# Kernel optimization log

Hardware: AMD Instinct MI355X
Metric: run time of the kernel (lower is better)

The kernel has to match this reference:

```python
import jax, jax.numpy as jnp
import numpy as np

E = 200_000   # edges (messages)
T = 2_000_000 # triplets
N = 20_000    # atoms/nodes
H = 128       # hidden_channels
INT = 64      # int_emb_size
BAS = 8       # basis_emb_size
OUT_EMB = 256 # out_emb_channels
NRAD = 6
SBF_DIM = 7 * 6  # num_spherical * num_radial = 42
NB = 4        # num_blocks
OUTC = 1      # num_targets


def setup_inputs() -> dict:
    key = jax.random.key(0)
    ks = iter(jax.random.split(key, 64))

    def w(shape):
        # glorot-ish scaled weights, stored as [in, out] for x @ W
        return jax.random.normal(next(ks), shape, jnp.float32) / np.sqrt(shape[-2])

    return dict(
        x=jax.random.normal(next(ks), (E, H), jnp.float32),
        rbf=jax.random.normal(next(ks), (E, NRAD), jnp.float32),
        sbf=jax.random.normal(next(ks), (T, SBF_DIM), jnp.float32),
        # interaction block params, stacked over NB blocks
        W_rbf1=w((NB, NRAD, BAS)), W_rbf2=w((NB, BAS, H)),
        W_sbf1=w((NB, SBF_DIM, BAS)), W_sbf2=w((NB, BAS, INT)),
        W_kj=w((NB, H, H)), b_kj=jnp.zeros((NB, H), jnp.float32),
        W_ji=w((NB, H, H)), b_ji=jnp.zeros((NB, H), jnp.float32),
        W_down=w((NB, H, INT)), W_up=w((NB, INT, H)),
        Wb=w((NB, 2, H, H)), bb=jnp.zeros((NB, 2, H), jnp.float32),   # num_before_skip=1 -> 2 linears
        Wa=w((NB, 4, H, H)), ba=jnp.zeros((NB, 4, H), jnp.float32),   # num_after_skip=2 -> 4 linears
        W_lin=w((NB, H, H)), b_lin=jnp.zeros((NB, H), jnp.float32),
        # output block params, stacked over NB+1 blocks
        Wo_rbf=w((NB + 1, NRAD, H)),
        Wo_up=w((NB + 1, H, OUT_EMB)), bo_up=jnp.zeros((NB + 1, OUT_EMB), jnp.float32),
        Wo_lins=w((NB + 1, 3, OUT_EMB, OUT_EMB)), bo_lins=jnp.zeros((NB + 1, 3, OUT_EMB), jnp.float32),
        Wo_out=w((NB + 1, OUT_EMB, OUTC)),
        idx_kj=jax.random.randint(next(ks), (T,), 0, E, jnp.int32),
        idx_ji=jax.random.randint(next(ks), (T,), 0, E, jnp.int32),
        idx_i=jax.random.randint(next(ks), (E,), 0, N, jnp.int32),
        num_nodes=N,
    )


def _interaction(b, x, rbf, sbf, idx_kj, idx_ji, p):
    act = jax.nn.silu
    x_ji = act(x @ p['W_ji'][b] + p['b_ji'][b])
    x_kj = act(x @ p['W_kj'][b] + p['b_kj'][b])
    rbf_t = (rbf @ p['W_rbf1'][b]) @ p['W_rbf2'][b]          # [E,H]
    x_kj = act((x_kj * rbf_t) @ p['W_down'][b])              # [E,INT]
    sbf_t = (sbf @ p['W_sbf1'][b]) @ p['W_sbf2'][b]          # [T,INT]
    m = x_kj[idx_kj] * sbf_t                                  # triplet gather [T,INT]
    agg = jax.ops.segment_sum(m, idx_ji, num_segments=x.shape[0])  # scatter-add [E,INT]
    x_kj = act(agg @ p['W_up'][b])                            # [E,H]
    h = x_ji + x_kj
    # residual layers before skip (1 layer = 2 linears)
    h = h + act(act(h @ p['Wb'][b, 0] + p['bb'][b, 0]) @ p['Wb'][b, 1] + p['bb'][b, 1])
    h = act(h @ p['W_lin'][b] + p['b_lin'][b]) + x
    # residual layers after skip (2 layers = 4 linears)
    for l in range(2):
        h = h + act(act(h @ p['Wa'][b, 2 * l] + p['ba'][b, 2 * l]) @ p['Wa'][b, 2 * l + 1] + p['ba'][b, 2 * l + 1])
    return h


def _output(b, x, rbf, idx_i, num_nodes, p):
    act = jax.nn.silu
    t = (rbf @ p['Wo_rbf'][b]) * x                            # [E,H]
    t = jax.ops.segment_sum(t, idx_i, num_segments=num_nodes) # [N,H]
    t = t @ p['Wo_up'][b] + p['bo_up'][b]
    for l in range(3):
        t = act(t @ p['Wo_lins'][b, l] + p['bo_lins'][b, l])
    return t @ p['Wo_out'][b]                                 # [N,OUTC]


def reference(x, rbf, sbf, W_rbf1, W_rbf2, W_sbf1, W_sbf2, W_kj, b_kj, W_ji, b_ji,
              W_down, W_up, Wb, bb, Wa, ba, W_lin, b_lin,
              Wo_rbf, Wo_up, bo_up, Wo_lins, bo_lins, Wo_out,
              idx_kj, idx_ji, idx_i, num_nodes):
    p = dict(W_rbf1=W_rbf1, W_rbf2=W_rbf2, W_sbf1=W_sbf1, W_sbf2=W_sbf2,
             W_kj=W_kj, b_kj=b_kj, W_ji=W_ji, b_ji=b_ji, W_down=W_down, W_up=W_up,
             Wb=Wb, bb=bb, Wa=Wa, ba=ba, W_lin=W_lin, b_lin=b_lin,
             Wo_rbf=Wo_rbf, Wo_up=Wo_up, bo_up=bo_up,
             Wo_lins=Wo_lins, bo_lins=bo_lins, Wo_out=Wo_out)
    P = _output(0, x, rbf, idx_i, num_nodes, p)
    for b in range(NB):  # fixed small layer loop
        x = _interaction(b, x, rbf, sbf, idx_kj, idx_ji, p)
        P = P + _output(b + 1, x, rbf, idx_i, num_nodes, p)
    return P
```

## Files before the change

kernel.cpp:

```cpp
#include <hip/hip_runtime.h>
#include <hip/hip_bf16.h>

#define E_EDGES 200000
#define T_TRIP  2000000
#define N_NODES 20000
#define H_DIM   128
#define INT_DIM 64
#define BAS     8
#define OUT_EMB 256
#define NRAD    6
#define SBF_D   42
#define NB      4

typedef __attribute__((ext_vector_type(8))) __bf16 bf16x8;
typedef __attribute__((ext_vector_type(4))) float f32x4;
typedef unsigned short u16;

__device__ __forceinline__ float silu_f(float v) { return v / (1.0f + __expf(-v)); }

__device__ __forceinline__ u16 f2bf(float f) {
    unsigned int u = __float_as_uint(f);
    u += 0x7FFF + ((u >> 16) & 1);
    return (u16)(u >> 16);
}
// ... 75 lines not shown
{
    __builtin_amdgcn_s_setprio(1);
    #pragma unroll
    for (int m = 0; m < 2; ++m) {
        int row = wm * 32 + m * 16 + l15;
        int off = (row * 256 + (k0 + khalf) * 2) ^ ((row & 7) << 4);
        bf16x8 ah = *reinterpret_cast<const bf16x8*>(AH + off);
        bf16x8 al = *reinterpret_cast<const bf16x8*>(AL + off);
        #pragma unroll
        for (int n = 0; n < 4; ++n) {
            acc[m][n] = __builtin_amdgcn_mfma_f32_16x16x32_bf16(b.h[n], ah, acc[m][n], 0, 0, 0);
            acc[m][n] = __builtin_amdgcn_mfma_f32_16x16x32_bf16(b.h[n], al, acc[m][n], 0, 0, 0);
            acc[m][n] = __builtin_amdgcn_mfma_f32_16x16x32_bf16(b.l[n], ah, acc[m][n], 0, 0, 0);
        }
    }
    __builtin_amdgcn_s_setprio(0);
}
__device__ __forceinline__ void mfma_cluster_T(
    const char* T, int k0, int wm, int l15, int khalf,
    const BF8x4& b, f32x4 acc[2][4])
{
    __builtin_amdgcn_s_setprio(1);
    #pragma unroll
    for (int m = 0; m < 2; ++m) {
        int row = wm * 32 + m * 16 + l15;
        int off = (row * 256 + (k0 + khalf) * 2) ^ ((row & 7) << 4);
        bf16x8 a = *reinterpret_cast<const bf16x8*>(T + off);
        #pragma unroll
        for (int n = 0; n < 4; ++n) {
            acc[m][n] = __builtin_amdgcn_mfma_f32_16x16x32_bf16(b.h[n], a, acc[m][n], 0, 0, 0);
            acc[m][n] = __builtin_amdgcn_mfma_f32_16x16x32_bf16(b.l[n], a, acc[m][n], 0, 0, 0);
        }
    }
    __builtin_amdgcn_s_setprio(0);
}
__device__ __forceinline__ void mfma_cluster64_T(
    const char* T, int k0, int wm, int l15, int khalf,
    const BF8x4& b, f32x4 acc[2][4])
{
    __builtin_amdgcn_s_setprio(1);
    #pragma unroll
    for (int m = 0; m < 2; ++m) {
        int row = wm * 32 + m * 16 + l15;
        int off = (row * 128 + (k0 + khalf) * 2) ^ ((row & 7) << 4);
        bf16x8 a = *reinterpret_cast<const bf16x8*>(T + off);
        #pragma unroll
        for (int n = 0; n < 4; ++n) {
            acc[m][n] = __builtin_amdgcn_mfma_f32_16x16x32_bf16(b.h[n], a, acc[m][n], 0, 0, 0);
            acc[m][n] = __builtin_amdgcn_mfma_f32_16x16x32_bf16(b.l[n], a, acc[m][n], 0, 0, 0);
        }
    }
    __builtin_amdgcn_s_setprio(0);
}
__device__ __forceinline__ void mfma_cluster512(
    const char* AH, const char* AL, int k0, int l15, int khalf,
    const BF8x4& b, f32x4 acc[2][4])
{
    __builtin_amdgcn_s_setprio(1);
    #pragma unroll
    for (int m = 0; m < 2; ++m) {
        int row = m * 16 + l15;
        int off = (row * 512 + (k0 + khalf) * 2) ^ ((row & 7) << 4);
        bf16x8 ah = *reinterpret_cast<const bf16x8*>(AH + off);
        bf16x8 al = *reinterpret_cast<const bf16x8*>(AL + off);
        #pragma unroll
        for (int n = 0; n < 4; ++n) {
            acc[m][n] = __builtin_amdgcn_mfma_f32_16x16x32_bf16(b.h[n], ah, acc[m][n], 0, 0, 0);
            acc[m][n] = __builtin_amdgcn_mfma_f32_16x16x32_bf16(b.h[n], al, acc[m][n], 0, 0, 0);
            acc[m][n] = __builtin_amdgcn_mfma_f32_16x16x32_bf16(b.l[n], ah, acc[m][n], 0, 0, 0);
        }
    }
    __builtin_amdgcn_s_setprio(0);
}
__device__ __forceinline__ void mfma_cluster512_T(
    const char* T, int k0, int l15, int khalf,
    const BF8x4& b, f32x4 acc[2][4])
{
    __builtin_amdgcn_s_setprio(1);
    #pragma unroll
    for (int m = 0; m < 2; ++m) {
        int row = m * 16 + l15;
        int off = (row * 512 + (k0 + khalf) * 2) ^ ((row & 7) << 4);
        bf16x8 a = *reinterpret_cast<const bf16x8*>(T + off);
        #pragma unroll
        for (int n = 0; n < 4; ++n) {
            acc[m][n] = __builtin_amdgcn_mfma_f32_16x16x32_bf16(b.h[n], a, acc[m][n], 0, 0, 0);
            acc[m][n] = __builtin_amdgcn_mfma_f32_16x16x32_bf16(b.l[n], a, acc[m][n], 0, 0, 0);
        }
    }
    __builtin_amdgcn_s_setprio(0);
}

__device__ __forceinline__ void mm128_pipe(
    const char* AH, const char* AL,
    const u16* __restrict__ Bh, const u16* __restrict__ Bl, BF8x4& pre,
    const u16* __restrict__ nBh, const u16* __restrict__ nBl,
    int wm, int wn, int l15, int khalf, f32x4 acc[2][4])
{
    BF8x4 c0 = pre;
    BF8x4 c1 = loadB128f(Bh, Bl, 32, wn, l15, khalf);
    mfma_cluster(AH, AL, 0, wm, l15, khalf, c0, acc);
    BF8x4 c2 = loadB128f(Bh, Bl, 64, wn, l15, khalf);
    mfma_cluster(AH, AL, 32, wm, l15, khalf, c1, acc);
    BF8x4 c3 = loadB128f(Bh, Bl, 96, wn, l15, khalf);
    mfma_cluster(AH, AL, 64, wm, l15, khalf, c2, acc);
    if (nBh) pre = loadB128f(nBh, nBl, 0, wn, l15, khalf);
    mfma_cluster(AH, AL, 96, wm, l15, khalf, c3, acc);
}
__device__ __forceinline__ void mm128_pipe_T(
    const char* T,
    const u16* __restrict__ Bh, const u16* __restrict__ Bl, BF8x4& pre,
    const u16* __restrict__ nBh, const u16* __restrict__ nBl,
    int wm, int wn, int l15, int khalf, f32x4 acc[2][4])
{
    BF8x4 c0 = pre;
    BF8x4 c1 = loadB128f(Bh, Bl, 32, wn, l15, khalf);
    mfma_cluster_T(T, 0, wm, l15, khalf, c0, acc);
    BF8x4 c2 = loadB128f(Bh, Bl, 64, wn, l15, khalf);
    mfma_cluster_T(T, 32, wm, l15, khalf, c1, acc);
    BF8x4 c3 = loadB128f(Bh, Bl, 96, wn, l15, khalf);
    mfma_cluster_T(T, 64, wm, l15, khalf, c2, acc);
    if (nBh) pre = loadB128f(nBh, nBl, 0, wn, l15, khalf);
    mfma_cluster_T(T, 96, wm, l15, khalf, c3, acc);
}
__device__ __forceinline__ void mm64_pipe_T(
    const char* T,
    const u16* __restrict__ Bh, const u16* __restrict__ Bl, BF8x4& pre,
    const u16* __restrict__ nBh, const u16* __restrict__ nBl,
    int wm, int wn, int l15, int khalf, f32x4 acc[2][4])
{
    BF8x4 c0 = pre;
    BF8x4 c1 = loadB64f(Bh, Bl, 32, wn, l15, khalf);
    mfma_cluster64_T(T, 0, wm, l15, khalf, c0, acc);
    if (nBh) pre = loadB128f(nBh, nBl, 0, wn, l15, khalf);
    mfma_cluster64_T(T, 32, wm, l15, khalf, c1, acc);
}

__global__ __launch_bounds__(256) void wprep(
    const float* __restrict__ src, u16* __restrict__ hi,
    u16* __restrict__ lo, int K, int N)
{
    int e = blockIdx.x * 256 + threadIdx.x;
    int total = K * N;
    if (e >= total) return;
    size_t base = (size_t)blockIdx.y * total;
    float a = src[base + e];
    int k = e / N, n = e - k * N;
    u16 h = f2bf(a);
    u16 l = f2bf(a - bf2f(h));
    hi[base + (size_t)n * K + k] = h;
    lo[base + (size_t)n * K + k] = l;
}

__global__ __launch_bounds__(256, 2) void pre_fuse(
    const float* __restrict__ X, const float* __restrict__ rbf,
    const float* __restrict__ W1,
    const u16* __restrict__ Wjih, const u16* __restrict__ Wjil, const float* __restrict__ bji,
    const u16* __restrict__ Wkjh, const u16* __restrict__ Wkjl, const float* __restrict__ bkj,
    const float* __restrict__ Wr2,
    const u16* __restrict__ Wdnh, const u16* __restrict__ Wdnl,
    u16* __restrict__ E1, u16* __restrict__ C1)
{
    __shared__ char smem[49152];
    char* XH = smem;
    char* XL = smem + 16384;
    char* IT = smem + 32768;

    const int tid  = threadIdx.x;
    const int lane = tid & 63;
    const int w    = tid >> 6;
    const int wm   = w >> 1, wn = w & 1;
    const int bm   = blockIdx.x * 64;
    const int l15  = lane & 15;
    const int khalf = (lane >> 4) * 8;
    const int r4   = (lane >> 4) * 4;

    BF8x4 pre = loadB128f(Wjih, Wjil, 0, wn, l15, khalf);

    {
        int r  = tid >> 2;
        int c0 = (tid & 3) * 32;
        const float* p = &X[(size_t)(bm + r) * H_DIM + c0];
        const int swz = (r & 7) << 4;
        #pragma unroll
        for (int q = 0; q < 8; ++q) {
            float4 f = *reinterpret_cast<const float4*>(p + q * 4);
            float vv[4] = {f.x, f.y, f.z, f.w};
            u16 h[4], l[4];
            #pragma unroll
            for (int j = 0; j < 4; ++j) {
                h[j] = f2bf(vv[j]);
                l[j] = f2bf(vv[j] - bf2f(h[j]));
            }
            int off = (r * 256 + c0 * 2 + q * 8) ^ swz;
            *reinterpret_cast<ushort4*>(XH + off) = make_ushort4(h[0], h[1], h[2], h[3]);
            *reinterpret_cast<ushort4*>(XL + off) = make_ushort4(l[0], l[1], l[2], l[3]);
        }
    }
    __syncthreads();

    {
        f32x4 acc[2][4] = {};
        mm128_pipe(XH, XL, Wjih, Wjil, pre, Wkjh, Wkjl, wm, wn, l15, khalf, acc);
        #pragma unroll
        for (int n = 0; n < 4; ++n) {
            int col0 = wn * 64 + n * 16 + r4;
            float4 bv = *reinterpret_cast<const float4*>(&bji[col0]);
            #pragma unroll
            for (int m = 0; m < 2; ++m) {
                int row = wm * 32 + m * 16 + l15;
                ushort4 ob;
                ob.x = f2bf(silu_f(acc[m][n][0] + bv.x));
                ob.y = f2bf(silu_f(acc[m][n][1] + bv.y));
                ob.z = f2bf(silu_f(acc[m][n][2] + bv.z));
                ob.w = f2bf(silu_f(acc[m][n][3] + bv.w));
                *reinterpret_cast<ushort4*>(&E1[(size_t)(bm + row) * H_DIM + col0]) = ob;
            }
        }
    }
    {
        f32x4 acc[2][4] = {};
        mm128_pipe(XH, XL, Wkjh, Wkjl, pre, nullptr, nullptr, wm, wn, l15, khalf, acc);
        float r8v[2][8];
        #pragma unroll
        for (int m = 0; m < 2; ++m) {
            int grow = bm + wm * 32 + m * 16 + l15;
            const float2* rp = reinterpret_cast<const float2*>(&rbf[(size_t)grow * NRAD]);
            float2 q0 = rp[0], q1 = rp[1], q2 = rp[2];
            float rv[NRAD] = {q0.x, q0.y, q1.x, q1.y, q2.x, q2.y};
            #pragma unroll
            for (int j = 0; j < 8; ++j) r8v[m][j] = 0.f;
            #pragma unroll
            for (int k = 0; k < NRAD; ++k)
                #pragma unroll
                for (int j = 0; j < 8; ++j)
                    r8v[m][j] = fmaf(rv[k], W1[k * BAS + j], r8v[m][j]);
        }
        #pragma unroll
        for (int n = 0; n < 4; ++n) {
            int col0 = wn * 64 + n * 16 + r4;
            float4 bvf = *reinterpret_cast<const float4*>(&bkj[col0]);
            float bv[4] = {bvf.x, bvf.y, bvf.z, bvf.w};
            float wrv[8][4];
            #pragma unroll
            for (int j = 0; j < 8; ++j) {
                float4 wf = *reinterpret_cast<const float4*>(&Wr2[j * H_DIM + col0]);
                wrv[j][0] = wf.x; wrv[j][1] = wf.y; wrv[j][2] = wf.z; wrv[j][3] = wf.w;
            }
            #pragma unroll
            for (int m = 0; m < 2; ++m) {
                int row = wm * 32 + m * 16 + l15;
                float v[4];
                #pragma unroll
                for (int r = 0; r < 4; ++r) {
                    float t = silu_f(acc[m][n][r] + bv[r]);
                    float g = 0.f;
                    #pragma unroll
                    for (int j = 0; j < 8; ++j)
                        g = fmaf(r8v[m][j], wrv[j][r], g);
                    v[r] = t * g;
                }
                st_bf4(IT, row, col0, 256, v);
            }
        }
    }
    __syncthreads();

    {
        f32x4 acc[2][2] = {};
        #pragma unroll
        for (int k0 = 0; k0 < 128; k0 += 32) {
            bf16x8 bh[2], bl[2];
            #pragma unroll
            for (int n = 0; n < 2; ++n) {
                size_t bo = (size_t)(wn * 32 + n * 16 + l15) * 128 + k0 + khalf;
                bh[n] = *reinterpret_cast<const bf16x8*>(Wdnh + bo);
                bl[n] = *reinterpret_cast<const bf16x8*>(Wdnl + bo);
            }
            __builtin_amdgcn_s_setprio(1);
            #pragma unroll
            for (int m = 0; m < 2; ++m) {
                int row = wm * 32 + m * 16 + l15;
                int off = (row * 256 + (k0 + khalf) * 2) ^ ((row & 7) << 4);
                bf16x8 a = *reinterpret_cast<const bf16x8*>(IT + off);
                #pragma unroll
                for (int n = 0; n < 2; ++n) {
                    acc[m][n] = __builtin_amdgcn_mfma_f32_16x16x32_bf16(bh[n], a, acc[m][n], 0, 0, 0);
                    acc[m][n] = __builtin_amdgcn_mfma_f32_16x16x32_bf16(bl[n], a, acc[m][n], 0, 0, 0);
                }
            }
            __builtin_amdgcn_s_setprio(0);
        }
        #pragma unroll
        for (int n = 0; n < 2; ++n) {
            int col0 = wn * 32 + n * 16 + r4;
            #pragma unroll
            for (int m = 0; m < 2; ++m) {
                int row = wm * 32 + m * 16 + l15;
                ushort4 ob;
                ob.x = f2bf(silu_f(acc[m][n][0]));
                ob.y = f2bf(silu_f(acc[m][n][1]));
                ob.z = f2bf(silu_f(acc[m][n][2]));
                ob.w = f2bf(silu_f(acc[m][n][3]));
                *reinterpret_cast<ushort4*>(&C1[(size_t)(bm + row) * INT_DIM + col0]) = ob;
            }
        }
    }
}

struct ChainP {
    const u16 *uph, *upl;
    const u16 *b0h, *b0l, *b1h, *b1l;
    const u16 *lnh, *lnl;
    const u16 *a0h, *a0l, *a1h, *a1l, *a2h, *a2l, *a3h, *a3l;
    const float *bb0, *bb1, *blin, *ba0, *ba1, *ba2, *ba3;
};
struct OutP {
    const float* TN;
    const u16 *Uh, *Ul; const float* bu;
    const u16 *L0h, *L0l; const float* b0;
    const u16 *L1h, *L1l; const float* b1;
    const u16 *L2h, *L2l; const float* b2;
    const float* Wo; float* P;
};

__device__ __forceinline__ void post_chain_body(
    char* smem, int bx,
    const u16* __restrict__ AGG, const u16* __restrict__ E1,
    const float* __restrict__ X, const ChainP& p, float* __restrict__ OUT)
{
    char* SH  = smem;
    char* SL  = smem + 16384;
    char* TMP = smem + 32768;
    char* GB  = TMP;

    const int tid  = threadIdx.x;
    const int lane = tid & 63;
    const int w    = tid >> 6;
    const int wm   = w >> 1, wn = w & 1;
    const int bm   = bx * 64;
    const int l15  = lane & 15;
    const int khalf = (lane >> 4) * 8;
    const int r4   = (lane >> 4) * 4;

    BF8x4 pre = loadB64f(p.uph, p.upl, 0, wn, l15, khalf);

    {
        int r  = tid >> 2;
        int c0 = (tid & 3) * 16;
        const ushort4* pg = reinterpret_cast<const ushort4*>(&AGG[(size_t)(bm + r) * INT_DIM + c0]);
        const int swz = (r & 7) << 4;
        #pragma unroll
        for (int q = 0; q < 4; ++q) {
            ushort4 v = pg[q];
            int off = (r * 128 + c0 * 2 + q * 8) ^ swz;
            *reinterpret_cast<ushort4*>(GB + off) = v;
        }
    }
    __syncthreads();

    f32x4 acc[2][4];
    #define ZACC { _Pragma("unroll") for (int m = 0; m < 2; ++m) \
                   _Pragma("unroll") for (int n = 0; n < 4; ++n) \
                       acc[m][n] = f32x4{0.f, 0.f, 0.f, 0.f}; }

    ZACC
    mm64_pipe_T(GB, p.uph, p.upl, pre, p.b0h, p.b0l, wm, wn, l15, khalf, acc);
    #pragma unroll
    for (int n = 0; n < 4; ++n) {
        int col0 = wn * 64 + n * 16 + r4;
        #pragma unroll
        for (int m = 0; m < 2; ++m) {
            int row = wm * 32 + m * 16 + l15;
            ushort4 e = *reinterpret_cast<const ushort4*>(&E1[(size_t)(bm + row) * H_DIM + col0]);
            float v[4];
            v[0] = bf2f(e.x) + silu_f(acc[m][n][0]);
            v[1] = bf2f(e.y) + silu_f(acc[m][n][1]);
            v[2] = bf2f(e.z) + silu_f(acc[m][n][2]);
            v[3] = bf2f(e.w) + silu_f(acc[m][n][3]);
            st_split4(SH, SL, row, col0, 256, v);
        }
    }
    __syncthreads();

    #define STAGE_PLAIN(WH, WL, BIAS, NWH, NWL)                                         \
    {                                                                                   \
        ZACC                                                                            \
        mm128_pipe(SH, SL, WH, WL, pre, NWH, NWL, wm, wn, l15, khalf, acc);             \
        _Pragma("unroll")                                                               \
        for (int n = 0; n < 4; ++n) {                                                   \
            int col0 = wn * 64 + n * 16 + r4;                                           \
            float4 bv = *reinterpret_cast<const float4*>(&BIAS[col0]);                  \
            _Pragma("unroll")                                                           \
            for (int m = 0; m < 2; ++m) {                                               \
                int row = wm * 32 + m * 16 + l15;                                       \
                float v[4];                                                             \
                v[0] = silu_f(acc[m][n][0] + bv.x);                                     \
                v[1] = silu_f(acc[m][n][1] + bv.y);                                     \
                v[2] = silu_f(acc[m][n][2] + bv.z);                                     \
                v[3] = silu_f(acc[m][n][3] + bv.w);                                     \
                st_bf4(TMP, row, col0, 256, v);                                         \
            }                                                                           \
        }                                                                               \
        __syncthreads();                                                                \
    }

    #define STAGE_RES(WH, WL, BIAS, NWH, NWL)                                           \
    {                                                                                   \
        ZACC                                                                            \
        mm128_pipe_T(TMP, WH, WL, pre, NWH, NWL, wm, wn, l15, khalf, acc);              \
        _Pragma("unroll")                                                               \
        for (int n = 0; n < 4; ++n) {                                                   \
            int col0 = wn * 64 + n * 16 + r4;                                           \
            float4 bv = *reinterpret_cast<const float4*>(&BIAS[col0]);                  \
            _Pragma("unroll")                                                           \
            for (int m = 0; m < 2; ++m) {                                               \
                int row = wm * 32 + m * 16 + l15;                                       \
                float v[4];                                                             \
                ld_split4(SH, SL, row, col0, 256, v);                                   \
                v[0] += silu_f(acc[m][n][0] + bv.x);                                    \
                v[1] += silu_f(acc[m][n][1] + bv.y);                                    \
                v[2] += silu_f(acc[m][n][2] + bv.z);                                    \
                v[3] += silu_f(acc[m][n][3] + bv.w);                                    \
                st_split4(SH, SL, row, col0, 256, v);                                   \
            }                                                                           \
        }                                                                               \
        __syncthreads();                                                                \
    }

    STAGE_PLAIN(p.b0h, p.b0l, p.bb0, p.b1h, p.b1l)
    STAGE_RES(p.b1h, p.b1l, p.bb1, p.lnh, p.lnl)

    {
        ZACC
        mm128_pipe(SH, SL, p.lnh, p.lnl, pre, p.a0h, p.a0l, wm, wn, l15, khalf, acc);
        __syncthreads();
        #pragma unroll
        for (int n = 0; n < 4; ++n) {
            int col0 = wn * 64 + n * 16 + r4;
            float4 bv = *reinterpret_cast<const float4*>(&p.blin[col0]);
            #pragma unroll
            for (int m = 0; m < 2; ++m) {
                int row = wm * 32 + m * 16 + l15;
                float4 xv = *reinterpret_cast<const float4*>(&X[(size_t)(bm + row) * H_DIM + col0]);
                float v[4];
                v[0] = silu_f(acc[m][n][0] + bv.x) + xv.x;
                v[1] = silu_f(acc[m][n][1] + bv.y) + xv.y;
                v[2] = silu_f(acc[m][n][2] + bv.z) + xv.z;
                v[3] = silu_f(acc[m][n][3] + bv.w) + xv.w;
                st_split4(SH, SL, row, col0, 256, v);
            }
        }
        __syncthreads();
    }

    STAGE_PLAIN(p.a0h, p.a0l, p.ba0, p.a1h, p.a1l)
    STAGE_RES(p.a1h, p.a1l, p.ba1, p.a2h, p.a2l)
    STAGE_PLAIN(p.a2h, p.a2l, p.ba2, p.a3h, p.a3l)

    {
        ZACC
        mm128_pipe_T(TMP, p.a3h, p.a3l, pre, nullptr, nullptr, wm, wn, l15, khalf, acc);
        #pragma unroll
        for (int n = 0; n < 4; ++n) {
            int col0 = wn * 64 + n * 16 + r4;
            float4 bv = *reinterpret_cast<const float4*>(&p.ba3[col0]);
            #pragma unroll
            for (int m = 0; m < 2; ++m) {
                int row = wm * 32 + m * 16 + l15;
                float v[4];
                ld_split4(SH, SL, row, col0, 256, v);
                float4 o;
                o.x = v[0] + silu_f(acc[m][n][0] + bv.x);
                o.y = v[1] + silu_f(acc[m][n][1] + bv.y);
                o.z = v[2] + silu_f(acc[m][n][2] + bv.z);
                o.w = v[3] + silu_f(acc[m][n][3] + bv.w);
                *reinterpret_cast<float4*>(&OUT[(size_t)(bm + row) * H_DIM + col0]) = o;
            }
        }
    }
    #undef STAGE_PLAIN
    #undef STAGE_RES
    #undef ZACC
}

__device__ __forceinline__ void out_chain_body(char* smem, int bx, const OutP& o)
{
    char* SH  = smem;
    char* SL  = smem + 16384;
    char* TMP = smem + 32768;
    char* XH  = TMP;
    char* XL  = TMP + 8192;

    const int tid  = threadIdx.x;
    const int lane = tid & 63;
    const int wn   = tid >> 6;
    const int bm   = bx * 32;
    const int l15  = lane & 15;
    const int khalf = (lane >> 4) * 8;
    const int r4   = (lane >> 4) * 4;

    {
        int r  = tid >> 3;
        int c0 = (tid & 7) * 16;
        const float* p = &o.TN[(size_t)(bm + r) * H_DIM + c0];
        const int swz = (r & 7) << 4;
        #pragma unroll
        for (int q = 0; q < 4; ++q) {
            float4 f = *reinterpret_cast<const float4*>(p + q * 4);
            float vv[4] = {f.x, f.y, f.z, f.w};
            u16 h[4], l[4];
            #pragma unroll
            for (int j = 0; j < 4; ++j) {
                h[j] = f2bf(vv[j]);
                l[j] = f2bf(vv[j] - bf2f(h[j]));
            }
            int off = (r * 256 + c0 * 2 + q * 8) ^ swz;
            *reinterpret_cast<ushort4*>(XH + off) = make_ushort4(h[0], h[1], h[2], h[3]);
            *reinterpret_cast<ushort4*>(XL + off) = make_ushort4(l[0], l[1], l[2], l[3]);
        }
    }
    __syncthreads();

    f32x4 acc[2][4];
    #define ZACC { _Pragma("unroll") for (int m = 0; m < 2; ++m) \
                   _Pragma("unroll") for (int n = 0; n < 4; ++n) \
                       acc[m][n] = f32x4{0.f, 0.f, 0.f, 0.f}; }

    {
        ZACC
        BF8x4 cur = loadB128f(o.Uh, o.Ul, 0, wn, l15, khalf);
        #pragma unroll
        for (int k = 0; k < 4; ++k) {
            BF8x4 nxt;
            if (k < 3) nxt = loadB128f(o.Uh, o.Ul, 32 * (k + 1), wn, l15, khalf);
            mfma_cluster(XH, XL, 32 * k, 0, l15, khalf, cur, acc);
            if (k < 3) cur = nxt;
        }
        __syncthreads();
        #pragma unroll
        for (int n = 0; n < 4; ++n) {
            int col0 = wn * 64 + n * 16 + r4;
            float4 bv = *reinterpret_cast<const float4*>(&o.bu[col0]);
            #pragma unroll
            for (int m = 0; m < 2; ++m) {
                int row = m * 16 + l15;
                float v[4] = {acc[m][n][0] + bv.x, acc[m][n][1] + bv.y,
                              acc[m][n][2] + bv.z, acc[m][n][3] + bv.w};
                st_split4(SH, SL, row, col0, 512, v);
            }
        }
        __syncthreads();
    }

    {
        ZACC
        BF8x4 cur = loadB256f(o.L0h, o.L0l, 0, wn, l15, khalf);
        #pragma unroll
        for (int k = 0; k < 8; ++k) {
            BF8x4 nxt;
            if (k < 7) nxt = loadB256f(o.L0h, o.L0l, 32 * (k + 1), wn, l15, khalf);
            mfma_cluster512(SH, SL, 32 * k, l15, khalf, cur, acc);
            if (k < 7) cur = nxt;
        }
        #pragma unroll
        for (int n = 0; n < 4; ++n) {
            int col0 = wn * 64 + n * 16 + r4;
            float4 bv = *reinterpret_cast<const float4*>(&o.b0[col0]);
            #pragma unroll
            for (int m = 0; m < 2; ++m) {
                int row = m * 16 + l15;
                float v[4];
                v[0] = silu_f(acc[m][n][0] + bv.x);
                v[1] = silu_f(acc[m][n][1] + bv.y);
                v[2] = silu_f(acc[m][n][2] + bv.z);
                v[3] = silu_f(acc[m][n][3] + bv.w);
                st_bf4(TMP, row, col0, 512, v);
            }
        }
        __syncthreads();
    }

    {
        ZACC
        BF8x4 cur = loadB256f(o.L1h, o.L1l, 0, wn, l15, khalf);
        #pragma unroll
        for (int k = 0; k < 8; ++k) {
            BF8x4 nxt;
            if (k < 7) nxt = loadB256f(o.L1h, o.L1l, 32 * (k + 1), wn, l15, khalf);
            mfma_cluster512_T(TMP, 32 * k, l15, khalf, cur, acc);
            if (k < 7) cur = nxt;
        }
        #pragma unroll
        for (int n = 0; n < 4; ++n) {
            int col0 = wn * 64 + n * 16 + r4;
            float4 bv = *reinterpret_cast<const float4*>(&o.b1[col0]);
            #pragma unroll
            for (int m = 0; m < 2; ++m) {
                int row = m * 16 + l15;
                float v[4];
                v[0] = silu_f(acc[m][n][0] + bv.x);
                v[1] = silu_f(acc[m][n][1] + bv.y);
                v[2] = silu_f(acc[m][n][2] + bv.z);
                v[3] = silu_f(acc[m][n][3] + bv.w);
                st_split4(SH, SL, row, col0, 512, v);
            }
        }
        __syncthreads();
    }

    {
        ZACC
        BF8x4 cur = loadB256f(o.L2h, o.L2l, 0, wn, l15, khalf);
        #pragma unroll
        for (int k = 0; k < 8; ++k) {
            BF8x4 nxt;
            if (k < 7) nxt = loadB256f(o.L2h, o.L2l, 32 * (k + 1), wn, l15, khalf);
            mfma_cluster512(SH, SL, 32 * k, l15, khalf, cur, acc);
            if (k < 7) cur = nxt;
        }
        __syncthreads();
        #pragma unroll
        for (int n = 0; n < 4; ++n) {
            int col0 = wn * 64 + n * 16 + r4;
            float4 bv = *reinterpret_cast<const float4*>(&o.b2[col0]);
            #pragma unroll
            for (int m = 0; m < 2; ++m) {
                int row = m * 16 + l15;
                float v[4];
                v[0] = silu_f(acc[m][n][0] + bv.x);
                v[1] = silu_f(acc[m][n][1] + bv.y);
                v[2] = silu_f(acc[m][n][2] + bv.z);
                v[3] = silu_f(acc[m][n][3] + bv.w);
                st_split4(SH, SL, row, col0, 512, v);
            }
        }
        __syncthreads();
    }

    {
        int row  = tid >> 3;
        int part = tid & 7;
        float s = 0.f;
        int cbase = part * 32;
        #pragma unroll
        for (int c4 = 0; c4 < 32; c4 += 4) {
            float v[4];
            ld_split4(SH, SL, row, cbase + c4, 512, v);
            float4 wv = *reinterpret_cast<const float4*>(&o.Wo[cbase + c4]);
            s = fmaf(v[0], wv.x, s);
            s = fmaf(v[1], wv.y, s);
            s = fmaf(v[2], wv.z, s);
            s = fmaf(v[3], wv.w, s);
        }
        s += __shfl_xor(s, 1);
        s += __shfl_xor(s, 2);
        s += __shfl_xor(s, 4);
        if (part == 0) o.P[bm + row] += s;
    }
    #undef ZACC
}

__global__ __launch_bounds__(256, 2) void post_fused(
    int npost,
    const u16* __restrict__ AGG, const u16* __restrict__ E1,
    const float* __restrict__ X, ChainP p, float* __restrict__ OUT, OutP o)
{
    __shared__ char smem[49152];
    if ((int)blockIdx.x < npost)
        post_chain_body(smem, blockIdx.x, AGG, E1, X, p, OUT);
    else
        out_chain_body(smem, blockIdx.x - npost, o);
}

__device__ __forceinline__ float dot8_bf(uint4 r, const float* w2) {
    float s;
    s  = bf2f((u16)(r.x)) * w2[0] + bf2f((u16)(r.x >> 16)) * w2[1];
    s += bf2f((u16)(r.y)) * w2[2] + bf2f((u16)(r.y >> 16)) * w2[3];
    s += bf2f((u16)(r.z)) * w2[4] + bf2f((u16)(r.z >> 16)) * w2[5];
    s += bf2f((u16)(r.w)) * w2[6] + bf2f((u16)(r.w >> 16)) * w2[7];
    return s;
}

__device__ __forceinline__ void triplet_body(
    int bx, int nblk,
    const u16* __restrict__ ps8b, const float* __restrict__ Wsb2,
    const u16* __restrict__ xkj, const int* __restrict__ pkj,
    const int* __restrict__ tptr, const int* __restrict__ tcnt,
    u16* __restrict__ agg)
{
    const int lane = threadIdx.x & 63;
    int wid = bx * 4 + (threadIdx.x >> 6);
    const int nw = nblk * 4;
    float w2[BAS];
    #pragma unroll
    for (int j = 0; j < BAS; ++j) w2[j] = Wsb2[j * INT_DIM + lane];

    for (int e = wid; e < E_EDGES; e += nw) {
        int start = tptr[e];
        int end   = start + tcnt[e];
        float acc0 = 0.f, acc1 = 0.f;
        int i = start;
        for (; i + 1 < end; i += 2) {
            uint4 ra = *reinterpret_cast<const uint4*>(&ps8b[(size_t)i * BAS]);
            uint4 rb = *reinterpret_cast<const uint4*>(&ps8b[(size_t)(i + 1) * BAS]);
            int e0 = pkj[i], e1 = pkj[i + 1];
            float s0 = dot8_bf(ra, w2);
            float s1 = dot8_bf(rb, w2);
            acc0 = fmaf(bf2f(xkj[(size_t)e0 * INT_DIM + lane]), s0, acc0);
            acc1 = fmaf(bf2f(xkj[(size_t)e1 * INT_DIM + lane]), s1, acc1);
        }
        if (i < end) {
            uint4 ra = *reinterpret_cast<const uint4*>(&ps8b[(size_t)i * BAS]);
            int e0 = pkj[i];
            acc0 = fmaf(bf2f(xkj[(size_t)e0 * INT_DIM + lane]), dot8_bf(ra, w2), acc0);
        }
        agg[(size_t)e * INT_DIM + lane] = f2bf(acc0 + acc1);
    }
}

__device__ __forceinline__ void out_gather_body(
    int bx, int nblk,
    const float* __restrict__ rbf, const float* __restrict__ Wor,
    const float* __restrict__ x,
    const int* __restrict__ eptr, const int* __restrict__ ecnt,
    const int* __restrict__ eperm, float* __restrict__ tN)
{
    const int lane = threadIdx.x & 63;
    int wid = bx * 4 + (threadIdx.x >> 6);
    const int nw = nblk * 4;
    float wr0[NRAD], wr1[NRAD];
    #pragma unroll
    for (int k = 0; k < NRAD; ++k) {
        wr0[k] = Wor[k * H_DIM + lane];
        wr1[k] = Wor[k * H_DIM + lane + 64];
    }
    for (int n = wid; n < N_NODES; n += nw) {
        int start = eptr[n];
        int end   = start + ecnt[n];
        float a0 = 0.f, a1 = 0.f;
        for (int i = start; i < end; ++i) {
            int e = eperm[i];
            const float2* rp = reinterpret_cast<const float2*>(&rbf[(size_t)e * NRAD]);
            float2 r0 = rp[0], r1 = rp[1], r2 = rp[2];
            float rA = r0.x*wr0[0] + r0.y*wr0[1] + r1.x*wr0[2]
                     + r1.y*wr0[3] + r2.x*wr0[4] + r2.y*wr0[5];
            float rB = r0.x*wr1[0] + r0.y*wr1[1] + r1.x*wr1[2]
                     + r1.y*wr1[3] + r2.x*wr1[4] + r2.y*wr1[5];
            a0 = fmaf(rA, x[(size_t)e * H_DIM + lane], a0);
            a1 = fmaf(rB, x[(size_t)e * H_DIM + lane + 64], a1);
        }
        tN[(size_t)n * H_DIM + lane] = a0;
        tN[(size_t)n * H_DIM + lane + 64] = a1;
    }
}

__global__ __launch_bounds__(256) void gather_fused(
    int GT,
    const u16* __restrict__ ps8b, const float* __restrict__ Wsb2,
    const u16* __restrict__ xkj, const int* __restrict__ pkj,
    const int* __restrict__ tptr, const int* __restrict__ tcnt,
    u16* __restrict__ agg,
    const float* __restrict__ rbf, const float* __restrict__ Wor,
    const float* __restrict__ x,
    const int* __restrict__ eptr, const int* __restrict__ ecnt,
    const int* __restrict__ eperm, float* __restrict__ tN)
{
    int bx = blockIdx.x;
    if (bx < GT)
        triplet_body(bx, GT, ps8b, Wsb2, xkj, pkj, tptr, tcnt, agg);
    else
        out_gather_body(bx - GT, gridDim.x - GT, rbf, Wor, x, eptr, ecnt, eperm, tN);
}

__global__ __launch_bounds__(256) void csr_count(
    const int* __restrict__ idx, int* __restrict__ cnt, int n)
{
    int i = blockIdx.x * 256 + threadIdx.x;
    if (i < n) atomicAdd(&cnt[idx[i]], 1);
}

__global__ __launch_bounds__(256) void scan_block(
    const int* __restrict__ cnt, int* __restrict__ ptr, int* __restrict__ bsum, int n)
{
    __shared__ int s[256];
    int i = blockIdx.x * 256 + threadIdx.x;
    int v = (i < n) ? cnt[i] : 0;
    s[threadIdx.x] = v;
    __syncthreads();
    #pragma unroll
    for (int off = 1; off < 256; off <<= 1) {
        int t = (threadIdx.x >= off) ? s[threadIdx.x - off] : 0;
        __syncthreads();
        s[threadIdx.x] += t;
        __syncthreads();
    }
    if (i < n) ptr[i] = s[threadIdx.x] - v;
    if (threadIdx.x == 255) bsum[blockIdx.x] = s[255];
}

__global__ __launch_bounds__(1024) void scan_aux(int* __restrict__ bsum, int nb)
{
    __shared__ int s[1024];
    int v = (threadIdx.x < nb) ? bsum[threadIdx.x] : 0;
    s[threadIdx.x] = v;
    __syncthreads();
    #pragma unroll
    for (int off = 1; off < 1024; off <<= 1) {
        int t = (threadIdx.x >= off) ? s[threadIdx.x - off] : 0;
        __syncthreads();
        s[threadIdx.x] += t;
        __syncthreads();
    }
    if (threadIdx.x < nb) bsum[threadIdx.x] = s[threadIdx.x] - v;
}

__global__ __launch_bounds__(256) void scan_add(
    int* __restrict__ ptr, const int* __restrict__ bsum, int n)
{
    int i = blockIdx.x * 256 + threadIdx.x;
    if (i < n) ptr[i] += bsum[blockIdx.x];
}

__global__ __launch_bounds__(256) void csr_fill(
    const int* __restrict__ idx, int* __restrict__ cursor,
    int* __restrict__ perm, int n)
{
    int i = blockIdx.x * 256 + threadIdx.x;
    if (i >= n) return;
    int pos = atomicAdd(&cursor[idx[i]], 1);
    perm[pos] = i;
}

__global__ __launch_bounds__(256) void permute_s8(
    const float* __restrict__ sbf, const float* __restrict__ W1all,
    const int* __restrict__ idx_kj, const int* __restrict__ tperm,
    u16* __restrict__ ps8, int* __restrict__ pkj, int Tcount)
{
    __shared__ float Ws[NB * SBF_D * BAS];
    for (int i = threadIdx.x; i < NB * SBF_D * BAS; i += 256) Ws[i] = W1all[i];
    __syncthreads();
    int i = blockIdx.x * 256 + threadIdx.x;
    if (i >= Tcount) return;
    int t = tperm[i];
    pkj[i] = idx_kj[t];
    float s[SBF_D];
    {
        const float2* p2 = reinterpret_cast<const float2*>(&sbf[(size_t)t * SBF_D]);
        #pragma unroll
        for (int k = 0; k < SBF_D / 2; ++k) {
            float2 v = p2[k];
            s[2 * k] = v.x; s[2 * k + 1] = v.y;
        }
    }
    #pragma unroll
    for (int b = 0; b < NB; ++b) {
        const float* Wb_ = &Ws[b * SBF_D * BAS];
        float acc[BAS] = {};
        for (int k = 0; k < SBF_D; ++k) {
            float sv = s[k];
            #pragma unroll
            for (int j = 0; j < BAS; ++j)
                acc[j] = fmaf(sv, Wb_[k * BAS + j], acc[j]);
        }
        ushort4 o0 = make_ushort4(f2bf(acc[0]), f2bf(acc[1]), f2bf(acc[2]), f2bf(acc[3]));
        ushort4 o1 = make_ushort4(f2bf(acc[4]), f2bf(acc[5]), f2bf(acc[6]), f2bf(acc[7]));
        u16* op = &ps8[((size_t)b * Tcount + i) * BAS];
        *reinterpret_cast<ushort4*>(op) = o0;
        *reinterpret_cast<ushort4*>(op + 4) = o1;
    }
}

extern "C" void kernel_launch(void* const* d_in, const int* in_sizes, int n_in,
                              void* d_out, int out_size, void* d_ws, size_t ws_size,
                              hipStream_t stream)
{
    const float* x_in    = (const float*)d_in[0];
    const float* rbf     = (const float*)d_in[1];
    const float* sbf     = (const float*)d_in[2];
    const float* W_rbf1  = (const float*)d_in[3];
    const float* W_rbf2  = (const float*)d_in[4];
    const float* W_sbf1  = (const float*)d_in[5];
    const float* W_sbf2  = (const float*)d_in[6];
    const float* W_kj    = (const float*)d_in[7];
    const float* b_kj    = (const float*)d_in[8];
    const float* W_ji    = (const float*)d_in[9];
    const float* b_ji    = (const float*)d_in[10];
    const float* W_down  = (const float*)d_in[11];
    const float* W_up    = (const float*)d_in[12];
    const float* Wb      = (const float*)d_in[13];
    const float* bb      = (const float*)d_in[14];
    const float* Wa      = (const float*)d_in[15];
    const float* ba      = (const float*)d_in[16];
    const float* W_lin   = (const float*)d_in[17];
    const float* b_lin   = (const float*)d_in[18];
    const float* Wo_rbf  = (const float*)d_in[19];
    const float* Wo_up   = (const float*)d_in[20];
    const float* bo_up   = (const float*)d_in[21];
    const float* Wo_lins = (const float*)d_in[22];
    const float* bo_lins = (const float*)d_in[23];
    const float* Wo_out  = (const float*)d_in[24];
    const int*   idx_kj  = (const int*)d_in[25];
    const int*   idx_ji  = (const int*)d_in[26];
    const int*   idx_i   = (const int*)d_in[27];

    char* ws = (char*)d_ws;
    size_t off = 0;
    auto alloc = [&](size_t bytes) -> void* {
        void* p = (void*)(ws + off);
        off += (bytes + 255) & ~(size_t)255;
        return p;
    };
    float* XA  = (float*)alloc((size_t)E_EDGES * H_DIM * 4);
    float* XB  = (float*)alloc((size_t)E_EDGES * H_DIM * 4);
    u16*   E1B = (u16*)alloc((size_t)E_EDGES * H_DIM * 2);
    u16*   C1B = (u16*)alloc((size_t)E_EDGES * INT_DIM * 2);
    u16*   C2B = (u16*)alloc((size_t)E_EDGES * INT_DIM * 2);
    float* TN  = (float*)alloc((size_t)N_NODES * H_DIM * 4);
    u16* HKJ = (u16*)alloc(4  * 16384 * 2); u16* LKJ = (u16*)alloc(4  * 16384 * 2);
    u16* HJI = (u16*)alloc(4  * 16384 * 2); u16* LJI = (u16*)alloc(4  * 16384 * 2);
    u16* HDN = (u16*)alloc(4  * 8192  * 2); u16* LDN = (u16*)alloc(4  * 8192  * 2);
    u16* HUP = (u16*)alloc(4  * 8192  * 2); u16* LUP = (u16*)alloc(4  * 8192  * 2);
    u16* HWB = (u16*)alloc(8  * 16384 * 2); u16* LWB = (u16*)alloc(8  * 16384 * 2);
    u16* HWA = (u16*)alloc(16 * 16384 * 2); u16* LWA = (u16*)alloc(16 * 16384 * 2);
    u16* HLN = (u16*)alloc(4  * 16384 * 2); u16* LLN = (u16*)alloc(4  * 16384 * 2);
    u16* HOU = (u16*)alloc(5  * 32768 * 2); u16* LOU = (u16*)alloc(5  * 32768 * 2);
    u16* HOL = (u16*)alloc(15 * 65536 * 2); u16* LOL = (u16*)alloc(15 * 65536 * 2);
    int* tcnt  = (int*)alloc((size_t)E_EDGES * 4);
    int* tptr  = (int*)alloc((size_t)E_EDGES * 4);
    int* tcur  = (int*)alloc((size_t)E_EDGES * 4);
    int* tperm = (int*)alloc((size_t)T_TRIP * 4);
    int* tbsum = (int*)alloc(1024 * 4);
    int* ecnt  = (int*)alloc((size_t)N_NODES * 4);
    int* eptr  = (int*)alloc((size_t)N_NODES * 4);
    int* ecur  = (int*)alloc((size_t)N_NODES * 4);
    int* eperm = (int*)alloc((size_t)E_EDGES * 4);
    int* ebsum = (int*)alloc(1024 * 4);
    u16* PS8 = (u16*)alloc((size_t)NB * T_TRIP * BAS * 2);
    int* PKJ = (int*)alloc((size_t)T_TRIP * 4);
    (void)ws_size;

    auto prep = [&](const float* src, u16* hi, u16* lo, int K, int N, int cnt) {
        dim3 g((K * N + 255) / 256, cnt);
        hipLaunchKernelGGL(wprep, g, dim3(256), 0, stream, src, hi, lo, K, N);
    };
    prep(W_kj,    HKJ, LKJ, 128, 128, 4);
    prep(W_ji,    HJI, LJI, 128, 128, 4);
    prep(W_down,  HDN, LDN, 128, 64,  4);
    prep(W_up,    HUP, LUP, 64,  128, 4);
    prep(Wb,      HWB, LWB, 128, 128, 8);
    prep(Wa,      HWA, LWA, 128, 128, 16);
    prep(W_lin,   HLN, LLN, 128, 128, 4);
    prep(Wo_up,   HOU, LOU, 128, 256, 5);
    prep(Wo_lins, HOL, LOL, 256, 256, 15);

    {
        const int nbT = (E_EDGES + 255) / 256;
        hipMemsetAsync(tcnt, 0, (size_t)E_EDGES * 4, stream);
        hipLaunchKernelGGL(csr_count, dim3((T_TRIP + 255) / 256), dim3(256), 0, stream,
                           idx_ji, tcnt, T_TRIP);
        hipLaunchKernelGGL(scan_block, dim3(nbT), dim3(256), 0, stream, tcnt, tptr, tbsum, E_EDGES);
        hipLaunchKernelGGL(scan_aux, dim3(1), dim3(1024), 0, stream, tbsum, nbT);
        hipLaunchKernelGGL(scan_add, dim3(nbT), dim3(256), 0, stream, tptr, tbsum, E_EDGES);
        hipMemcpyAsync(tcur, tptr, (size_t)E_EDGES * 4, hipMemcpyDeviceToDevice, stream);
        hipLaunchKernelGGL(csr_fill, dim3((T_TRIP + 255) / 256), dim3(256), 0, stream,
                           idx_ji, tcur, tperm, T_TRIP);
    }
    {
        const int nbN = (N_NODES + 255) / 256;
        hipMemsetAsync(ecnt, 0, (size_t)N_NODES * 4, stream);
        hipLaunchKernelGGL(csr_count, dim3((E_EDGES + 255) / 256), dim3(256), 0, stream,
                           idx_i, ecnt, E_EDGES);
        hipLaunchKernelGGL(scan_block, dim3(nbN), dim3(256), 0, stream, ecnt, eptr, ebsum, N_NODES);
        hipLaunchKernelGGL(scan_aux, dim3(1), dim3(1024), 0, stream, ebsum, nbN);
        hipLaunchKernelGGL(scan_add, dim3(nbN), dim3(256), 0, stream, eptr, ebsum, N_NODES);
        hipMemcpyAsync(ecur, eptr, (size_t)N_NODES * 4, hipMemcpyDeviceToDevice, stream);
        hipLaunchKernelGGL(csr_fill, dim3((E_EDGES + 255) / 256), dim3(256), 0, stream,
                           idx_i, ecur, eperm, E_EDGES);
    }
    hipLaunchKernelGGL(permute_s8, dim3((T_TRIP + 255) / 256), dim3(256), 0, stream,
                       sbf, W_sbf1, idx_kj, tperm, PS8, PKJ, T_TRIP);

    float* P = (float*)d_out;
    hipMemsetAsync(P, 0, (size_t)N_NODES * sizeof(float), stream);

    auto make_outp = [&](int ob) {
        OutP o;
        o.TN = TN;
        o.Uh = HOU + (size_t)ob * 32768; o.Ul = LOU + (size_t)ob * 32768;
        o.bu = bo_up + (size_t)ob * OUT_EMB;
        o.L0h = HOL + (size_t)(ob * 3 + 0) * 65536; o.L0l = LOL + (size_t)(ob * 3 + 0) * 65536;
        o.b0 = bo_lins + (size_t)(ob * 3 + 0) * OUT_EMB;
        o.L1h = HOL + (size_t)(ob * 3 + 1) * 65536; o.L1l = LOL + (size_t)(ob * 3 + 1) * 65536;
        o.b1 = bo_lins + (size_t)(ob * 3 + 1) * OUT_EMB;
        o.L2h = HOL + (size_t)(ob * 3 + 2) * 65536; o.L2l = LOL + (size_t)(ob * 3 + 2) * 65536;
        o.b2 = bo_lins + (size_t)(ob * 3 + 2) * OUT_EMB;
        o.Wo = Wo_out + (size_t)ob * OUT_EMB;
        o.P = P;
        return o;
    };

    const float* xcur = x_in;
    const int EB = E_EDGES / 64;
    const int GT = 2048;
    for (int b = 0; b < NB; ++b) {
        float* xnext = (b % 2 == 0) ? XB : XA;
        hipLaunchKernelGGL(pre_fuse, dim3(EB), dim3(256), 0, stream,
                           xcur, rbf, W_rbf1 + (size_t)b * NRAD * BAS,
                           HJI + (size_t)b * 16384, LJI + (size_t)b * 16384, b_ji + (size_t)b * H_DIM,
                           HKJ + (size_t)b * 16384, LKJ + (size_t)b * 16384, b_kj + (size_t)b * H_DIM,
                           W_rbf2 + (size_t)b * BAS * H_DIM,
                           HDN + (size_t)b * 8192, LDN + (size_t)b * 8192,
                           E1B, C1B);
        hipLaunchKernelGGL(gather_fused, dim3(GT + 2048), dim3(256), 0, stream,
                           GT,
                           PS8 + (size_t)b * T_TRIP * BAS, W_sbf2 + (size_t)b * BAS * INT_DIM,
                           C1B, PKJ, tptr, tcnt, C2B,
                           rbf, Wo_rbf + (size_t)b * NRAD * H_DIM, xcur,
                           eptr, ecnt, eperm, TN);
        ChainP cp;
        cp.uph = HUP + (size_t)b * 8192;  cp.upl = LUP + (size_t)b * 8192;
        cp.b0h = HWB + (size_t)(b * 2 + 0) * 16384; cp.b0l = LWB + (size_t)(b * 2 + 0) * 16384;
        cp.b1h = HWB + (size_t)(b * 2 + 1) * 16384; cp.b1l = LWB + (size_t)(b * 2 + 1) * 16384;
        cp.lnh = HLN + (size_t)b * 16384; cp.lnl = LLN + (size_t)b * 16384;
        cp.a0h = HWA + (size_t)(b * 4 + 0) * 16384; cp.a0l = LWA + (size_t)(b * 4 + 0) * 16384;
        cp.a1h = HWA + (size_t)(b * 4 + 1) * 16384; cp.a1l = LWA + (size_t)(b * 4 + 1) * 16384;
        cp.a2h = HWA + (size_t)(b * 4 + 2) * 16384; cp.a2l = LWA + (size_t)(b * 4 + 2) * 16384;
        cp.a3h = HWA + (size_t)(b * 4 + 3) * 16384; cp.a3l = LWA + (size_t)(b * 4 + 3) * 16384;
        cp.bb0 = bb + (size_t)(b * 2 + 0) * H_DIM;
        cp.bb1 = bb + (size_t)(b * 2 + 1) * H_DIM;
        cp.blin = b_lin + (size_t)b * H_DIM;
        cp.ba0 = ba + (size_t)(b * 4 + 0) * H_DIM;
        cp.ba1 = ba + (size_t)(b * 4 + 1) * H_DIM;
        cp.ba2 = ba + (size_t)(b * 4 + 2) * H_DIM;
        cp.ba3 = ba + (size_t)(b * 4 + 3) * H_DIM;
        OutP op = make_outp(b);
        hipLaunchKernelGGL(post_fused, dim3(EB + N_NODES / 32), dim3(256), 0, stream,
                           EB, C2B, E1B, xcur, cp, xnext, op);
        xcur = xnext;
    }
    {
        OutP op = make_outp(NB);
        ChainP cp = {};
        hipLaunchKernelGGL(gather_fused, dim3(2048), dim3(256), 0, stream,
                           0,
                           PS8, W_sbf2, C1B, PKJ, tptr, tcnt, C2B,
                           rbf, Wo_rbf + (size_t)NB * NRAD * H_DIM, xcur,
                           eptr, ecnt, eperm, TN);
        hipLaunchKernelGGL(post_fused, dim3(N_NODES / 32), dim3(256), 0, stream,
                           0, C2B, E1B, xcur, cp, (float*)XA, op);
    }
}
```

Measured before the change: 3.990 ms.

## Store inter-block edge features in bf16 and drop split-precision X operand

The edge hidden state x passed between interaction blocks is now stored as bf16 instead of fp32. A new conversion kernel casts the input once, and pre_fuse uses a single-bf16 A operand (mm128_pipe_T) instead of the hi/lo split. This halves x read/write traffic in pre_fuse, post_fused and the output gather, cuts LDS in pre_fuse, and removes part of the split-precision MFMA work. In exchange, the residual state loses precision, which compounds across blocks and may push the result past tolerance.

```diff
diff --git a/kernel.cpp b/kernel.cpp
--- a/kernel.cpp
+++ b/kernel.cpp
@@ -251,8 +251,19 @@
     lo[base + (size_t)n * K + k] = l;
 }
 
+__global__ __launch_bounds__(256) void cvt_bf(
+    const float* __restrict__ src, u16* __restrict__ dst, int n4)
+{
+    int i = blockIdx.x * 256 + threadIdx.x;
+    if (i >= n4) return;
+    float4 f = *reinterpret_cast<const float4*>(&src[(size_t)i * 4]);
+    ushort4 o;
+    o.x = f2bf(f.x); o.y = f2bf(f.y); o.z = f2bf(f.z); o.w = f2bf(f.w);
+    *reinterpret_cast<ushort4*>(&dst[(size_t)i * 4]) = o;
+}
+
 __global__ __launch_bounds__(256, 2) void pre_fuse(
-    const float* __restrict__ X, const float* __restrict__ rbf,
+    const u16* __restrict__ X, const float* __restrict__ rbf,
     const float* __restrict__ W1,
     const u16* __restrict__ Wjih, const u16* __restrict__ Wjil, const float* __restrict__ bji,
     const u16* __restrict__ Wkjh, const u16* __restrict__ Wkjl, const float* __restrict__ bkj,
@@ -260,10 +271,9 @@
     const u16* __restrict__ Wdnh, const u16* __restrict__ Wdnl,
     u16* __restrict__ E1, u16* __restrict__ C1)
 {
-    __shared__ char smem[49152];
-    char* XH = smem;
-    char* XL = smem + 16384;
-    char* IT = smem + 32768;
+    __shared__ char smem[32768];
+    char* XT = smem;
+    char* IT = smem + 16384;
 
     const int tid  = threadIdx.x;
     const int lane = tid & 63;
@@ -279,28 +289,20 @@
     {
         int r  = tid >> 2;
         int c0 = (tid & 3) * 32;
-        const float* p = &X[(size_t)(bm + r) * H_DIM + c0];
+        const u16* p = &X[(size_t)(bm + r) * H_DIM + c0];
         const int swz = (r & 7) << 4;
         #pragma unroll
-        for (int q = 0; q < 8; ++q) {
-            float4 f = *reinterpret_cast<const float4*>(p + q * 4);
-            float vv[4] = {f.x, f.y, f.z, f.w};
-            u16 h[4], l[4];
-            #pragma unroll
-            for (int j = 0; j < 4; ++j) {
-                h[j] = f2bf(vv[j]);
-                l[j] = f2bf(vv[j] - bf2f(h[j]));
-            }
-            int off = (r * 256 + c0 * 2 + q * 8) ^ swz;
-            *reinterpret_cast<ushort4*>(XH + off) = make_ushort4(h[0], h[1], h[2], h[3]);
-            *reinterpret_cast<ushort4*>(XL + off) = make_ushort4(l[0], l[1], l[2], l[3]);
+        for (int q = 0; q < 4; ++q) {
+            uint4 v = *reinterpret_cast<const uint4*>(p + q * 8);
+            int off = (r * 256 + c0 * 2 + q * 16) ^ swz;
+            *reinterpret_cast<uint4*>(XT + off) = v;
         }
     }
     __syncthreads();
 
     {
         f32x4 acc[2][4] = {};
-        mm128_pipe(XH, XL, Wjih, Wjil, pre, Wkjh, Wkjl, wm, wn, l15, khalf, acc);
+        mm128_pipe_T(XT, Wjih, Wjil, pre, Wkjh, Wkjl, wm, wn, l15, khalf, acc);
         #pragma unroll
         for (int n = 0; n < 4; ++n) {
             int col0 = wn * 64 + n * 16 + r4;
@@ -319,7 +321,7 @@
     }
     {
         f32x4 acc[2][4] = {};
-        mm128_pipe(XH, XL, Wkjh, Wkjl, pre, nullptr, nullptr, wm, wn, l15, khalf, acc);
+        mm128_pipe_T(XT, Wkjh, Wkjl, pre, nullptr, nullptr, wm, wn, l15, khalf, acc);
         float r8v[2][8];
         #pragma unroll
         for (int m = 0; m < 2; ++m) {
@@ -335,6 +337,7 @@
                 for (int j = 0; j < 8; ++j)
                     r8v[m][j] = fmaf(rv[k], W1[k * BAS + j], r8v[m][j]);
         }
+        __syncthreads();
         #pragma unroll
         for (int n = 0; n < 4; ++n) {
             int col0 = wn * 64 + n * 16 + r4;
@@ -426,7 +429,7 @@
 __device__ __forceinline__ void post_chain_body(
     char* smem, int bx,
     const u16* __restrict__ AGG, const u16* __restrict__ E1,
-    const float* __restrict__ X, const ChainP& p, float* __restrict__ OUT)
+    const u16* __restrict__ X, const ChainP& p, u16* __restrict__ OUT)
 {
     char* SH  = smem;
     char* SL  = smem + 16384;
@@ -541,12 +544,12 @@
             #pragma unroll
             for (int m = 0; m < 2; ++m) {
                 int row = wm * 32 + m * 16 + l15;
-                float4 xv = *reinterpret_cast<const float4*>(&X[(size_t)(bm + row) * H_DIM + col0]);
+                ushort4 xv = *reinterpret_cast<const ushort4*>(&X[(size_t)(bm + row) * H_DIM + col0]);
                 float v[4];
-                v[0] = silu_f(acc[m][n][0] + bv.x) + xv.x;
-                v[1] = silu_f(acc[m][n][1] + bv.y) + xv.y;
-                v[2] = silu_f(acc[m][n][2] + bv.z) + xv.z;
-                v[3] = silu_f(acc[m][n][3] + bv.w) + xv.w;
+                v[0] = silu_f(acc[m][n][0] + bv.x) + bf2f(xv.x);
+                v[1] = silu_f(acc[m][n][1] + bv.y) + bf2f(xv.y);
+                v[2] = silu_f(acc[m][n][2] + bv.z) + bf2f(xv.z);
+                v[3] = silu_f(acc[m][n][3] + bv.w) + bf2f(xv.w);
                 st_split4(SH, SL, row, col0, 256, v);
             }
         }
@@ -569,12 +572,12 @@
                 int row = wm * 32 + m * 16 + l15;
                 float v[4];
                 ld_split4(SH, SL, row, col0, 256, v);
-                float4 o;
-                o.x = v[0] + silu_f(acc[m][n][0] + bv.x);
-                o.y = v[1] + silu_f(acc[m][n][1] + bv.y);
-                o.z = v[2] + silu_f(acc[m][n][2] + bv.z);
-                o.w = v[3] + silu_f(acc[m][n][3] + bv.w);
-                *reinterpret_cast<float4*>(&OUT[(size_t)(bm + row) * H_DIM + col0]) = o;
+                ushort4 ob;
+                ob.x = f2bf(v[0] + silu_f(acc[m][n][0] + bv.x));
+                ob.y = f2bf(v[1] + silu_f(acc[m][n][1] + bv.y));
+                ob.z = f2bf(v[2] + silu_f(acc[m][n][2] + bv.z));
+                ob.w = f2bf(v[3] + silu_f(acc[m][n][3] + bv.w));
+                *reinterpret_cast<ushort4*>(&OUT[(size_t)(bm + row) * H_DIM + col0]) = ob;
             }
         }
     }
@@ -763,7 +766,7 @@
 __global__ __launch_bounds__(256, 2) void post_fused(
     int npost,
     const u16* __restrict__ AGG, const u16* __restrict__ E1,
-    const float* __restrict__ X, ChainP p, float* __restrict__ OUT, OutP o)
+    const u16* __restrict__ X, ChainP p, u16* __restrict__ OUT, OutP o)
 {
     __shared__ char smem[49152];
     if ((int)blockIdx.x < npost)
@@ -821,7 +824,7 @@
 __device__ __forceinline__ void out_gather_body(
     int bx, int nblk,
     const float* __restrict__ rbf, const float* __restrict__ Wor,
-    const float* __restrict__ x,
+    const u16* __restrict__ x,
     const int* __restrict__ eptr, const int* __restrict__ ecnt,
     const int* __restrict__ eperm, float* __restrict__ tN)
 {
@@ -846,8 +849,8 @@
                      + r1.y*wr0[3] + r2.x*wr0[4] + r2.y*wr0[5];
             float rB = r0.x*wr1[0] + r0.y*wr1[1] + r1.x*wr1[2]
                      + r1.y*wr1[3] + r2.x*wr1[4] + r2.y*wr1[5];
-            a0 = fmaf(rA, x[(size_t)e * H_DIM + lane], a0);
-            a1 = fmaf(rB, x[(size_t)e * H_DIM + lane + 64], a1);
+            a0 = fmaf(rA, bf2f(x[(size_t)e * H_DIM + lane]), a0);
+            a1 = fmaf(rB, bf2f(x[(size_t)e * H_DIM + lane + 64]), a1);
         }
         tN[(size_t)n * H_DIM + lane] = a0;
         tN[(size_t)n * H_DIM + lane + 64] = a1;
@@ -861,7 +864,7 @@
     const int* __restrict__ tptr, const int* __restrict__ tcnt,
     u16* __restrict__ agg,
     const float* __restrict__ rbf, const float* __restrict__ Wor,
-    const float* __restrict__ x,
+    const u16* __restrict__ x,
     const int* __restrict__ eptr, const int* __restrict__ ecnt,
     const int* __restrict__ eperm, float* __restrict__ tN)
 {
@@ -1010,8 +1013,9 @@
         off += (bytes + 255) & ~(size_t)255;
         return p;
     };
-    float* XA  = (float*)alloc((size_t)E_EDGES * H_DIM * 4);
-    float* XB  = (float*)alloc((size_t)E_EDGES * H_DIM * 4);
+    u16*   X0B = (u16*)alloc((size_t)E_EDGES * H_DIM * 2);
+    u16*   XAB = (u16*)alloc((size_t)E_EDGES * H_DIM * 2);
+    u16*   XBB = (u16*)alloc((size_t)E_EDGES * H_DIM * 2);
     u16*   E1B = (u16*)alloc((size_t)E_EDGES * H_DIM * 2);
     u16*   C1B = (u16*)alloc((size_t)E_EDGES * INT_DIM * 2);
     u16*   C2B = (u16*)alloc((size_t)E_EDGES * INT_DIM * 2);
@@ -1053,6 +1057,9 @@
     prep(Wo_up,   HOU, LOU, 128, 256, 5);
     prep(Wo_lins, HOL, LOL, 256, 256, 15);
 
+    hipLaunchKernelGGL(cvt_bf, dim3((E_EDGES * H_DIM / 4 + 255) / 256), dim3(256), 0, stream,
+                       x_in, X0B, E_EDGES * H_DIM / 4);
+
     {
         const int nbT = (E_EDGES + 255) / 256;
         hipMemsetAsync(tcnt, 0, (size_t)E_EDGES * 4, stream);
@@ -1099,11 +1106,11 @@
         return o;
     };
 
-    const float* xcur = x_in;
+    const u16* xcur = X0B;
     const int EB = E_EDGES / 64;
     const int GT = 2048;
     for (int b = 0; b < NB; ++b) {
-        float* xnext = (b % 2 == 0) ? XB : XA;
+        u16* xnext = (b % 2 == 0) ? XAB : XBB;
         hipLaunchKernelGGL(pre_fuse, dim3(EB), dim3(256), 0, stream,
                            xcur, rbf, W_rbf1 + (size_t)b * NRAD * BAS,
                            HJI + (size_t)b * 16384, LJI + (size_t)b * 16384, b_ji + (size_t)b * H_DIM,
@@ -1147,6 +1154,6 @@
                            rbf, Wo_rbf + (size_t)NB * NRAD * H_DIM, xcur,
                            eptr, ecnt, eperm, TN);
         hipLaunchKernelGGL(post_fused, dim3(N_NODES / 32), dim3(256), 0, stream,
-                           0, C2B, E1B, xcur, cp, (float*)XA, op);
-    }
-}
+                           0, C2B, E1B, xcur, cp, XAB, op);
+    }
+}
```

New measurement: 3.890 ms. 1.03x faster.
